# Kernel optimization log

Hardware: AMD Instinct MI355X
Metric: run time of the kernel (lower is better)

Reference implementation:

```python
import jax, jax.numpy as jnp
import numpy as np

B, S, M = 8, 2048, 2048
STATE, MEM, DH, DOUT = 1024, 1024, 512, 512
K_CURV = 1.0
BETA = 1.0 / np.sqrt(DH)
EPS = 1e-12
MAX_TAN_NORM = 3.5


def setup_inputs() -> dict:
    key = jax.random.key(0)
    ks = jax.random.split(key, 6)
    return {
        "queries": jax.random.normal(ks[0], (B, S, STATE), jnp.float32),
        "keys": jax.random.normal(ks[1], (B, M, MEM), jnp.float32),
        "values": jax.random.normal(ks[2], (B, M, MEM), jnp.float32),
        "Wq": jax.random.normal(ks[3], (DH, STATE), jnp.float32) * (1.0 / np.sqrt(STATE)),
        "bq": jnp.zeros((DH,), jnp.float32),
        "Wk": jax.random.normal(ks[4], (DH, MEM), jnp.float32) * (1.0 / np.sqrt(MEM)),
        "bk": jnp.zeros((DH,), jnp.float32),
        "Wv": jax.random.normal(ks[5], (DOUT, MEM), jnp.float32) * (1.0 / np.sqrt(MEM)),
        "bv": jnp.zeros((DOUT,), jnp.float32),
    }


def _expmap0(x, k):
    # to_tangent0: [0, x] with norm clamped to <= 3.5 (time component is 0 so norm == ||x||)
    n = jnp.linalg.norm(x, axis=-1, keepdims=True)
    v = x * jnp.minimum(MAX_TAN_NORM / (n + 1e-7), 1.0)
    # exp map at origin o = (1/sqrt(k), 0) of Lorentz model with <x,x>_L = -1/k
    sk = jnp.sqrt(k)
    vn = jnp.maximum(jnp.linalg.norm(v, axis=-1, keepdims=True), EPS)
    th = sk * vn
    x0 = jnp.cosh(th) / sk
    xs = jnp.sinh(th) * v / (sk * vn)
    return jnp.concatenate([x0, xs], axis=-1)  # (..., d+1)


def _forward(queries, keys, values, Wq, bq, Wk, bk, Wv, bv):
    k = jnp.asarray(K_CURV, queries.dtype)
    sk = jnp.sqrt(k)
    Q = _expmap0(queries @ Wq.T + bq, k)  # (B,S,DH+1)
    Kh = _expmap0(keys @ Wk.T + bk, k)    # (B,M,DH+1)
    V = _expmap0(values @ Wv.T + bv, k)   # (B,M,DOUT+1)

    # pairwise Lorentz distance: d(x,y) = arccosh(-k <x,y>_L)/sqrt(k)
    # <x,y>_L = -x0*y0 + xs.ys ; computed as matmul + rank-1 term, no (B,S,M,d) blowup
    inner = jnp.einsum('bsd,bmd->bsm', Q[..., 1:], Kh[..., 1:]) \
            - Q[..., 0][:, :, None] * Kh[..., 0][:, None, :]
    dists = jnp.arccosh(jnp.maximum(-k * inner, 1.0 + 1e-7)) / sk  # (B,S,M)

    alpha = jax.nn.softmax(-BETA * dists, axis=-1)  # (B,S,M)

    # Einstein midpoint aggregation
    v_klein = V[..., 1:] / jnp.maximum(V[..., :1], EPS)                 # (B,M,DOUT)
    vn2 = jnp.minimum(jnp.sum(v_klein * v_klein, -1, keepdims=True), 1.0 - 1e-6)
    gamma = 1.0 / jnp.sqrt(jnp.maximum(1.0 - vn2, EPS))                 # (B,M,1)
    denom = jnp.maximum(jnp.einsum('bsm,bm->bs', alpha, gamma[..., 0]), EPS)[..., None]
    mid = jnp.einsum('bsm,bmd->bsd', alpha, gamma * v_klein) / denom    # (B,S,DOUT)
    mn = jnp.maximum(jnp.linalg.norm(mid, axis=-1, keepdims=True), EPS)
    mid = jnp.where(mn >= 1.0, mid / mn * (1.0 - 1e-6), mid)

    # Klein -> hyperboloid
    mn2 = jnp.minimum(jnp.sum(mid * mid, -1, keepdims=True), 1.0 - 1e-6)
    z0 = 1.0 / jnp.sqrt(jnp.maximum(k * (1.0 - mn2), EPS))
    zs = z0 * mid

    # logmap0 -> Euclidean spatial components
    d0 = jnp.arccosh(jnp.maximum(sk * z0, 1.0 + 1e-7)) / sk
    zsn = jnp.maximum(jnp.linalg.norm(zs, axis=-1, keepdims=True), EPS)
    return d0 * zs / zsn  # (B,S,DOUT)


def reference(queries, keys, values, Wq, bq, Wk, bk, Wv, bv):
    return _forward(queries, keys, values, Wq, bq, Wk, bk, Wv, bv)
```

## Files before the change

kernel.cpp:

```cpp
#include <hip/hip_runtime.h>
#include <hip/hip_bf16.h>
#include <cstdint>
#include <cstddef>


typedef _Float16 f16x8 __attribute__((ext_vector_type(8)));
typedef _Float16 f16x4 __attribute__((ext_vector_type(4)));
typedef float    f32x4 __attribute__((ext_vector_type(4)));

#define BETA_F 0.04419417382415922f
#define LOG2E_F 1.4426950408889634f
#define LN2_F 0.6931471805599453f

__device__ __forceinline__ void gload_lds16(const void* g, void* l) {
  __builtin_amdgcn_global_load_lds(
      (__attribute__((address_space(1))) void*)(g),
      (__attribute__((address_space(3))) void*)(l), 16, 0, 0);
}

#define K1_PIT 40

__global__ __launch_bounds__(256) void k_proj(
    const float* __restrict__ xq, const float* __restrict__ xk, const float* __restrict__ xv,
    const float* __restrict__ wq, const float* __restrict__ wk, const float* __restrict__ wv,
    const float* __restrict__ bq, const float* __restrict__ bk, const float* __restrict__ bv,
    _Float16* __restrict__ proj)
{
  __shared__ __align__(16) _Float16 As[128 * K1_PIT];
  __shared__ __align__(16) _Float16 Bs[128 * K1_PIT];

  const int tid = threadIdx.x;
  const int w = tid >> 6, l = tid & 63, ln = l & 15, q = l >> 4;
  const int wm = w & 1, wn = w >> 1;
  const int r0 = blockIdx.y * 128;
  const int n0 = blockIdx.x * 128;
  const int which = r0 >> 14;
  const int rloc = r0 & 16383;
  const float* X = (which == 0) ? xq : ((which == 1) ? xk : xv);
  const float* W = (which == 0) ? wq : ((which == 1) ? wk : wv);
  const float* bias = (which == 0) ? bq : ((which == 1) ? bk : bv);

  f32x4 acc[4][4];
#pragma unroll
  for (int mt = 0; mt < 4; ++mt)
#pragma unroll
    for (int nt = 0; nt < 4; ++nt) acc[mt][nt] = f32x4{0.f, 0.f, 0.f, 0.f};

  for (int kk = 0; kk < 1024; kk += 32) {
    __syncthreads();
#pragma unroll
    for (int it = 0; it < 4; ++it) {
      int v = tid + 256 * it;
      int row = v >> 3, c4 = v & 7;
      float4 a = *(const float4*)(X + (size_t)(rloc + row) * 1024 + kk + c4 * 4);
      float4 b = *(const float4*)(W + (size_t)(n0 + row) * 1024 + kk + c4 * 4);
      f16x4 ah = { (_Float16)a.x, (_Float16)a.y, (_Float16)a.z, (_Float16)a.w };
      f16x4 bh = { (_Float16)b.x, (_Float16)b.y, (_Float16)b.z, (_Float16)b.w };
      *(f16x4*)&As[row * K1_PIT + c4 * 4] = ah;
      *(f16x4*)&Bs[row * K1_PIT + c4 * 4] = bh;
    }
    __syncthreads();

    f16x8 af[4], bf[4];
#pragma unroll
    for (int mt = 0; mt < 4; ++mt)
      af[mt] = *(const f16x8*)&As[(wm * 64 + mt * 16 + ln) * K1_PIT + q * 8];
#pragma unroll
    for (int nt = 0; nt < 4; ++nt)
      bf[nt] = *(const f16x8*)&Bs[(wn * 64 + nt * 16 + ln) * K1_PIT + q * 8];
#pragma unroll
    for (int mt = 0; mt < 4; ++mt)
#pragma unroll
      for (int nt = 0; nt < 4; ++nt)
        acc[mt][nt] = __builtin_amdgcn_mfma_f32_16x16x32_f16(af[mt], bf[nt], acc[mt][nt], 0, 0, 0);
  }

  float bl[4];
#pragma unroll
  for (int nt = 0; nt < 4; ++nt) bl[nt] = bias[n0 + wn * 64 + nt * 16 + ln];
#pragma unroll
  for (int mt = 0; mt < 4; ++mt)
#pragma unroll
    for (int nt = 0; nt < 4; ++nt)
#pragma unroll
      for (int i = 0; i < 4; ++i) {
        int r = r0 + wm * 64 + mt * 16 + q * 4 + i;
        int c = n0 + wn * 64 + nt * 16 + ln;
        proj[(size_t)r * 512 + c] = (_Float16)(acc[mt][nt][i] + bl[nt]);
      }
}

__global__ __launch_bounds__(256) void k_rowstats(
    const _Float16* __restrict__ proj, float* __restrict__ fs, float* __restrict__ c0)
{
  const int w = threadIdx.x >> 6, l = threadIdx.x & 63;
  const int r = blockIdx.x * 4 + w;
  const f16x8 v = *(const f16x8*)(proj + (size_t)r * 512 + l * 8);
  float ss = 0.f;
#pragma unroll
  for (int j = 0; j < 8; ++j) { float x = (float)v[j]; ss += x * x; }
#pragma unroll
  for (int m = 1; m < 64; m <<= 1) ss += __shfl_xor(ss, m, 64);
  if (l == 0) {
    float n = sqrtf(ss);
    float s = fminf(3.5f / (n + 1e-7f), 1.0f);
    float vn = fmaxf(n * s, 1e-12f);
    float e = __builtin_amdgcn_exp2f(vn * LOG2E_F);
    float ie = 1.0f / e;
    c0[r] = 0.5f * (e + ie);
    fs[r] = 0.5f * (e - ie) * s / vn;
  }
}

#define K2_TP 72

__global__ __launch_bounds__(256) void k_transpose_v(
    const _Float16* __restrict__ proj, _Float16* __restrict__ xvT)
{
  __shared__ __align__(16) unsigned short t[64 * K2_TP];
  const int b = blockIdx.z, m0 = blockIdx.x * 64, d0 = blockIdx.y * 64;
  const unsigned short* pv =
      (const unsigned short*)(proj + (size_t)(32768 + b * 2048 + m0) * 512);
#pragma unroll
  for (int it = 0; it < 2; ++it) {
    int v = threadIdx.x + 256 * it;
    int r = v >> 3, c4 = v & 7;
    uint4 dd = *(const uint4*)(pv + (size_t)r * 512 + d0 + c4 * 8);
    *(uint4*)&t[r * K2_TP + c4 * 8] = dd;
  }
  __syncthreads();
#pragma unroll
  for (int it = 0; it < 2; ++it) {
    int v = threadIdx.x + 256 * it;
    int dr = v >> 3, mc = v & 7;
    unsigned int o[4];
#pragma unroll
    for (int jj = 0; jj < 4; ++jj) {
      unsigned int lo = t[(mc * 8 + jj * 2) * K2_TP + dr];
      unsigned int hi = t[(mc * 8 + jj * 2 + 1) * K2_TP + dr];
      o[jj] = lo | (hi << 16);
    }
    uint4 dd = { o[0], o[1], o[2], o[3] };
    unsigned short* dst =
        (unsigned short*)(xvT + ((size_t)b * 512 + d0 + dr) * 2048 + m0 + mc * 8);
    *(uint4*)dst = dd;
  }
}

__global__ __launch_bounds__(256, 2) void k_attn(
    const _Float16* __restrict__ proj, const _Float16* __restrict__ xvT,
    const float* __restrict__ fs, const float* __restrict__ c0,
    float* __restrict__ out)
{
  __shared__ __align__(16) _Float16 KV[16384];
  __shared__ __align__(16) _Float16 P[32 * 40];
  __shared__ float s_den[2][32];
  __shared__ float s_mn2[4][32];
  __shared__ float s_g[32];

  const int tid = threadIdx.x;
  const int w = tid >> 6, l = tid & 63, ln = l & 15, q = l >> 4;
  const int rh = w >> 1, ch = w & 1;
  const int b = blockIdx.y;
  const int s0 = blockIdx.x * 32;

  const _Float16* projq = proj + (size_t)(b * 2048 + s0) * 512;
  const _Float16* projk = proj + (size_t)(16384 + b * 2048) * 512;
  const _Float16* vt = xvT + (size_t)b * 512 * 2048;
  const float* fqp = fs + b * 2048 + s0;
  const float* fkp = fs + 16384 + b * 2048;
  const float* fvp = fs + 32768 + b * 2048;
  const float* cqp = c0 + b * 2048 + s0;
  const float* ckp = c0 + 16384 + b * 2048;
  const float* cvp = c0 + 32768 + b * 2048;

  f16x8 qf[16];
  {
    const _Float16* qrow = projq + (size_t)(rh * 16 + ln) * 512;
#pragma unroll
    for (int kc = 0; kc < 16; ++kc) qf[kc] = *(const f16x8*)(qrow + kc * 32 + q * 8);
  }
  float cq_i[4], fq_i[4];
#pragma unroll
  for (int i = 0; i < 4; ++i) {
    cq_i[i] = cqp[rh * 16 + q * 4 + i];
    fq_i[i] = fqp[rh * 16 + q * 4 + i];
  }

  f32x4 acc[2][8];
#pragma unroll
  for (int rt = 0; rt < 2; ++rt)
#pragma unroll
    for (int nt = 0; nt < 8; ++nt) acc[rt][nt] = f32x4{0.f, 0.f, 0.f, 0.f};
  float den_acc[4] = {0.f, 0.f, 0.f, 0.f};

  for (int m0 = 0; m0 < 2048; m0 += 32) {
    __syncthreads();
#pragma unroll
    for (int rr = 0; rr < 8; ++rr) {
      int mloc = w * 8 + rr;
      const _Float16* g = projk + (size_t)(m0 + mloc) * 512 + ((l ^ (mloc & 7)) * 8);
      gload_lds16(g, &KV[mloc * 512]);
    }
    const int mla = m0 + ch * 16 + ln;
    const float ck_v = ckp[mla], fk_v = fkp[mla], fv_v = fvp[mla], cv_v = cvp[mla];
    __syncthreads();

    f32x4 pacc = f32x4{0.f, 0.f, 0.f, 0.f};
    {
      const _Float16* krow = &KV[(ch * 16 + ln) * 512];
      const int msw = (ch * 16 + ln) & 7;
#pragma unroll
      for (int kc = 0; kc < 16; ++kc) {
        f16x8 kf = *(const f16x8*)(krow + (((kc * 4 + q) ^ msw) * 8));
        pacc = __builtin_amdgcn_mfma_f32_16x16x32_f16(qf[kc], kf, pacc, 0, 0, 0);
      }
    }
#pragma unroll
    for (int i = 0; i < 4; ++i) {
      float x = cq_i[i] * ck_v - (fq_i[i] * fk_v) * pacc[i];
      x = fmaxf(x, 1.0f + 1e-7f);
      float r_ = x + __builtin_amdgcn_sqrtf(x * x - 1.0f);
      float p = __builtin_amdgcn_exp2f(-BETA_F * __builtin_amdgcn_logf(r_));
      den_acc[i] += p * cv_v;
      P[(rh * 16 + q * 4 + i) * 40 + ch * 16 + ln] = (_Float16)(p * fv_v);
    }
    __syncthreads();
#pragma unroll
    for (int uu = 0; uu < 8; ++uu) {
      int u = w * 8 + uu;
      int dloc = u * 16 + (l >> 2);
      int cg = (l & 3) ^ ((dloc >> 1) & 3);
      const _Float16* g = vt + (size_t)dloc * 2048 + m0 + cg * 8;
      gload_lds16(g, &KV[u * 512]);
    }
    __syncthreads();
#pragma unroll
    for (int rt = 0; rt < 2; ++rt) {
      f16x8 pf = *(const f16x8*)&P[(rt * 16 + ln) * 40 + q * 8];
#pragma unroll
      for (int nt = 0; nt < 8; ++nt) {
        int d = w * 128 + nt * 16 + ln;
        f16x8 vf = *(const f16x8*)&KV[d * 32 + ((q ^ ((d >> 1) & 3)) * 8)];
        acc[rt][nt] = __builtin_amdgcn_mfma_f32_16x16x32_f16(pf, vf, acc[rt][nt], 0, 0, 0);
      }
    }
  }

#pragma unroll
  for (int i = 0; i < 4; ++i) {
    float v = den_acc[i];
    v += __shfl_xor(v, 1, 64); v += __shfl_xor(v, 2, 64);
    v += __shfl_xor(v, 4, 64); v += __shfl_xor(v, 8, 64);
    if (ln == 0) s_den[ch][rh * 16 + q * 4 + i] = v;
  }
  __syncthreads();
  if (tid < 32) {
    float dv = fmaxf(s_den[0][tid] + s_den[1][tid], 1e-12f);
    s_den[0][tid] = 1.0f / dv;
  }
  __syncthreads();
#pragma unroll
  for (int rt = 0; rt < 2; ++rt)
#pragma unroll
    for (int i = 0; i < 4; ++i) {
      int s = rt * 16 + q * 4 + i;
      float inv = s_den[0][s];
      float mm = 0.f;
#pragma unroll
      for (int nt = 0; nt < 8; ++nt) {
        float mid = acc[rt][nt][i] * inv;
        mm += mid * mid;
      }
      mm += __shfl_xor(mm, 1, 64); mm += __shfl_xor(mm, 2, 64);
      mm += __shfl_xor(mm, 4, 64); mm += __shfl_xor(mm, 8, 64);
      if (ln == 0) s_mn2[w][s] = mm;
    }
  __syncthreads();
  if (tid < 32) {
    float mn2 = s_mn2[0][tid] + s_mn2[1][tid] + s_mn2[2][tid] + s_mn2[3][tid];
    float mn = sqrtf(mn2);
    float sc = (mn >= 1.0f) ? (1.0f - 1e-6f) / mn : 1.0f;
    float mn2c = fminf(mn2 * sc * sc, 1.0f - 1e-6f);
    float z0 = 1.0f / sqrtf(fmaxf(1.0f - mn2c, 1e-12f));
    float zc = fmaxf(z0, 1.0f + 1e-7f);
    float d0 = LN2_F * __builtin_amdgcn_logf(zc + __builtin_amdgcn_sqrtf(zc * zc - 1.0f));
    s_g[tid] = (d0 / fmaxf(mn, 1e-12f)) * s_den[0][tid];
  }
  __syncthreads();

  float* pbuf = (float*)KV;
  for (int sp = 0; sp < 16; ++sp) {
#pragma unroll
    for (int rt = 0; rt < 2; ++rt)
#pragma unroll
      for (int i = 0; i < 4; ++i) {
        int s = rt * 16 + q * 4 + i;
        if ((s >> 1) == sp) {
          float gg = s_g[s];
#pragma unroll
          for (int nt = 0; nt < 8; ++nt)
            pbuf[(s & 1) * 512 + w * 128 + nt * 16 + ln] = gg * acc[rt][nt][i];
        }
      }
    __syncthreads();
    {
      int row = tid >> 7, c4 = tid & 127;
      float4 vv = *(float4*)&pbuf[row * 512 + c4 * 4];
      *(float4*)&out[((size_t)(b * 2048 + s0 + sp * 2 + row)) * 512 + c4 * 4] = vv;
    }
    __syncthreads();
  }
}

extern "C" void kernel_launch(void* const* d_in, const int* in_sizes, int n_in,
                              void* d_out, int out_size, void* d_ws, size_t ws_size,
                              hipStream_t stream) {
  (void)in_sizes; (void)n_in; (void)out_size; (void)ws_size;
  const float* xq = (const float*)d_in[0];
  const float* xk = (const float*)d_in[1];
  const float* xv = (const float*)d_in[2];
  const float* wq = (const float*)d_in[3];
  const float* bq = (const float*)d_in[4];
  const float* wk = (const float*)d_in[5];
  const float* bk = (const float*)d_in[6];
  const float* wv = (const float*)d_in[7];
  const float* bv = (const float*)d_in[8];
  float* out = (float*)d_out;
  char* ws = (char*)d_ws;

  _Float16* proj = (_Float16*)(ws);
  _Float16* xvT  = (_Float16*)(ws + 50331648);
  float* fsc     = (float*)(ws + 67108864);
  float* c0a     = (float*)(ws + 67305472);

  k_proj<<<dim3(4, 384), 256, 0, stream>>>(xq, xk, xv, wq, wk, wv, bq, bk, bv, proj);
  k_rowstats<<<dim3(12288), 256, 0, stream>>>(proj, fsc, c0a);
  k_transpose_v<<<dim3(32, 8, 8), 256, 0, stream>>>(proj, xvT);
  k_attn<<<dim3(64, 8), 256, 0, stream>>>(proj, xvT, fsc, c0a, out);
}
```

Measured before the change: 481.7 us.

## Split K and V staging buffers to overlap global loads with MFMA compute

Replaces the single shared K/V LDS buffer with two separate buffers. The V tile load is now issued before the QK^T MFMAs, and the next K tile is prefetched before the PV MFMAs, so global-to-LDS transfers run alongside compute instead of stalling behind barriers. The per-key scalars for the next tile are also loaded one iteration early. This doubles LDS use per block, which with two blocks per CU may limit occupancy.

```diff
diff --git a/kernel.cpp b/kernel.cpp
--- a/kernel.cpp
+++ b/kernel.cpp
@@ -152,7 +152,8 @@
     const float* __restrict__ fs, const float* __restrict__ c0,
     float* __restrict__ out)
 {
-  __shared__ __align__(16) _Float16 KV[16384];
+  __shared__ __align__(16) _Float16 KA[16384];
+  __shared__ __align__(16) _Float16 KB[16384];
   __shared__ __align__(16) _Float16 P[32 * 40];
   __shared__ float s_den[2][32];
   __shared__ float s_mn2[4][32];
@@ -174,6 +175,13 @@
   const float* ckp = c0 + 16384 + b * 2048;
   const float* cvp = c0 + 32768 + b * 2048;
 
+#pragma unroll
+  for (int rr = 0; rr < 8; ++rr) {
+    int mloc = w * 8 + rr;
+    const _Float16* g = projk + (size_t)mloc * 512 + ((l ^ (mloc & 7)) * 8);
+    gload_lds16(g, &KA[mloc * 512]);
+  }
+
   f16x8 qf[16];
   {
     const _Float16* qrow = projq + (size_t)(rh * 16 + ln) * 512;
@@ -186,6 +194,8 @@
     cq_i[i] = cqp[rh * 16 + q * 4 + i];
     fq_i[i] = fqp[rh * 16 + q * 4 + i];
   }
+  const int mll = ch * 16 + ln;
+  float ck_c = ckp[mll], fk_c = fkp[mll], fv_c = fvp[mll], cv_c = cvp[mll];
 
   f32x4 acc[2][8];
 #pragma unroll
@@ -195,36 +205,6 @@
   float den_acc[4] = {0.f, 0.f, 0.f, 0.f};
 
   for (int m0 = 0; m0 < 2048; m0 += 32) {
-    __syncthreads();
-#pragma unroll
-    for (int rr = 0; rr < 8; ++rr) {
-      int mloc = w * 8 + rr;
-      const _Float16* g = projk + (size_t)(m0 + mloc) * 512 + ((l ^ (mloc & 7)) * 8);
-      gload_lds16(g, &KV[mloc * 512]);
-    }
-    const int mla = m0 + ch * 16 + ln;
-    const float ck_v = ckp[mla], fk_v = fkp[mla], fv_v = fvp[mla], cv_v = cvp[mla];
-    __syncthreads();
-
-    f32x4 pacc = f32x4{0.f, 0.f, 0.f, 0.f};
-    {
-      const _Float16* krow = &KV[(ch * 16 + ln) * 512];
-      const int msw = (ch * 16 + ln) & 7;
-#pragma unroll
-      for (int kc = 0; kc < 16; ++kc) {
-        f16x8 kf = *(const f16x8*)(krow + (((kc * 4 + q) ^ msw) * 8));
-        pacc = __builtin_amdgcn_mfma_f32_16x16x32_f16(qf[kc], kf, pacc, 0, 0, 0);
-      }
-    }
-#pragma unroll
-    for (int i = 0; i < 4; ++i) {
-      float x = cq_i[i] * ck_v - (fq_i[i] * fk_v) * pacc[i];
-      x = fmaxf(x, 1.0f + 1e-7f);
-      float r_ = x + __builtin_amdgcn_sqrtf(x * x - 1.0f);
-      float p = __builtin_amdgcn_exp2f(-BETA_F * __builtin_amdgcn_logf(r_));
-      den_acc[i] += p * cv_v;
-      P[(rh * 16 + q * 4 + i) * 40 + ch * 16 + ln] = (_Float16)(p * fv_v);
-    }
     __syncthreads();
 #pragma unroll
     for (int uu = 0; uu < 8; ++uu) {
@@ -232,19 +212,53 @@
       int dloc = u * 16 + (l >> 2);
       int cg = (l & 3) ^ ((dloc >> 1) & 3);
       const _Float16* g = vt + (size_t)dloc * 2048 + m0 + cg * 8;
-      gload_lds16(g, &KV[u * 512]);
-    }
-    __syncthreads();
+      gload_lds16(g, &KB[u * 512]);
+    }
+    float ck_n = 0.f, fk_n = 0.f, fv_n = 0.f, cv_n = 0.f;
+    if (m0 + 32 < 2048) {
+      int mn = m0 + 32 + ch * 16 + ln;
+      ck_n = ckp[mn]; fk_n = fkp[mn]; fv_n = fvp[mn]; cv_n = cvp[mn];
+    }
+
+    f32x4 pacc = f32x4{0.f, 0.f, 0.f, 0.f};
+    {
+      const _Float16* krow = &KA[(ch * 16 + ln) * 512];
+      const int msw = (ch * 16 + ln) & 7;
+#pragma unroll
+      for (int kc = 0; kc < 16; ++kc) {
+        f16x8 kf = *(const f16x8*)(krow + (((kc * 4 + q) ^ msw) * 8));
+        pacc = __builtin_amdgcn_mfma_f32_16x16x32_f16(qf[kc], kf, pacc, 0, 0, 0);
+      }
+    }
+#pragma unroll
+    for (int i = 0; i < 4; ++i) {
+      float x = cq_i[i] * ck_c - (fq_i[i] * fk_c) * pacc[i];
+      x = fmaxf(x, 1.0f + 1e-7f);
+      float r_ = x + __builtin_amdgcn_sqrtf(x * x - 1.0f);
+      float p = __builtin_amdgcn_exp2f(-BETA_F * __builtin_amdgcn_logf(r_));
+      den_acc[i] += p * cv_c;
+      P[(rh * 16 + q * 4 + i) * 40 + ch * 16 + ln] = (_Float16)(p * fv_c);
+    }
+    __syncthreads();
+    if (m0 + 32 < 2048) {
+#pragma unroll
+      for (int rr = 0; rr < 8; ++rr) {
+        int mloc = w * 8 + rr;
+        const _Float16* g = projk + (size_t)(m0 + 32 + mloc) * 512 + ((l ^ (mloc & 7)) * 8);
+        gload_lds16(g, &KA[mloc * 512]);
+      }
+    }
 #pragma unroll
     for (int rt = 0; rt < 2; ++rt) {
       f16x8 pf = *(const f16x8*)&P[(rt * 16 + ln) * 40 + q * 8];
 #pragma unroll
       for (int nt = 0; nt < 8; ++nt) {
         int d = w * 128 + nt * 16 + ln;
-        f16x8 vf = *(const f16x8*)&KV[d * 32 + ((q ^ ((d >> 1) & 3)) * 8)];
+        f16x8 vf = *(const f16x8*)&KB[d * 32 + ((q ^ ((d >> 1) & 3)) * 8)];
         acc[rt][nt] = __builtin_amdgcn_mfma_f32_16x16x32_f16(pf, vf, acc[rt][nt], 0, 0, 0);
       }
     }
+    ck_c = ck_n; fk_c = fk_n; fv_c = fv_n; cv_c = cv_n;
   }
 
 #pragma unroll
@@ -289,7 +303,7 @@
   }
   __syncthreads();
 
-  float* pbuf = (float*)KV;
+  float* pbuf = (float*)KA;
   for (int sp = 0; sp < 16; ++sp) {
 #pragma unroll
     for (int rt = 0; rt < 2; ++rt)
```

New measurement: 465.2 us. 3.4% less time.
